# Performance work log

Hardware: AMD Instinct MI355X
Metric: run time of the kernel (lower is better)

## Reference

```python
import jax, jax.numpy as jnp
import numpy as np

N_NODES = 50000
N_EDGES = 800000
F_IN = 64
HID = 128
N_GRAPHS = 64
F_OUT = 1
NEG_SLOPE = 0.2


def _glorot(key, shape):
    fan_in, fan_out = shape[0], shape[-1]
    s = jnp.sqrt(6.0 / (fan_in + fan_out))
    return jax.random.uniform(key, shape, jnp.float32, -s, s)


def setup_inputs() -> dict:
    key = jax.random.key(0)
    ks = jax.random.split(key, 24)
    inp = {
        "x": jax.random.normal(ks[0], (N_NODES, F_IN), jnp.float32),
        "edge_index": jax.random.randint(ks[1], (2, N_EDGES), 0, N_NODES, jnp.int32),
        "edge_weight": jax.random.uniform(ks[2], (N_EDGES, 1), jnp.float32),
        "batch": jnp.sort(jax.random.randint(ks[3], (N_NODES,), 0, N_GRAPHS, jnp.int32)),
        # GATv2Conv layer 1 (heads=1): lin_l, lin_r (with bias), lin_edge (no bias), att, out-bias
        "W1l": _glorot(ks[4], (F_IN, HID)), "b1l": jnp.zeros((HID,), jnp.float32),
        "W1r": _glorot(ks[5], (F_IN, HID)), "b1r": jnp.zeros((HID,), jnp.float32),
        "We1": _glorot(ks[6], (1, HID)),
        "att1": _glorot(ks[7], (HID, 1))[:, 0],
        "bias1": jnp.zeros((HID,), jnp.float32),
        # GATv2Conv layer 2
        "W2l": _glorot(ks[8], (HID, HID)), "b2l": jnp.zeros((HID,), jnp.float32),
        "W2r": _glorot(ks[9], (HID, HID)), "b2r": jnp.zeros((HID,), jnp.float32),
        "We2": _glorot(ks[10], (1, HID)),
        "att2": _glorot(ks[11], (HID, 1))[:, 0],
        "bias2": jnp.zeros((HID,), jnp.float32),
        # final Linear
        "Wlin": _glorot(ks[12], (HID, F_OUT)),
        "blin": jnp.zeros((F_OUT,), jnp.float32),
    }
    return inp


def gatv2_layer(x, src, dst, eattr, Wl, bl, Wr, br, We, att, bias):
    n = x.shape[0]
    # add_self_loops=True with edge_attr fill_value='mean'
    loop = jnp.arange(n, dtype=src.dtype)
    src = jnp.concatenate([src, loop])
    dst = jnp.concatenate([dst, loop])
    mean_attr = jnp.mean(eattr, axis=0, keepdims=True)  # [1, edge_dim]
    eattr = jnp.concatenate([eattr, jnp.broadcast_to(mean_attr, (n, eattr.shape[1]))])
    xl = x @ Wl + bl            # [N, HID] source transform
    xr = x @ Wr + br            # [N, HID] dest transform
    ee = eattr @ We             # [E', HID] edge embedding
    m = jax.nn.leaky_relu(xl[src] + xr[dst] + ee, NEG_SLOPE)  # [E', HID]
    logits = m @ att            # [E']
    # per-destination softmax (every node has a self loop, so no empty segments)
    lmax = jax.ops.segment_max(logits, dst, num_segments=n)
    w = jnp.exp(logits - lmax[dst])
    denom = jax.ops.segment_sum(w, dst, num_segments=n)
    alpha = w / denom[dst]
    out = jax.ops.segment_sum(xl[src] * alpha[:, None], dst, num_segments=n)
    return out + bias


def reference(x, edge_index, edge_weight, batch,
              W1l, b1l, W1r, b1r, We1, att1, bias1,
              W2l, b2l, W2r, b2r, We2, att2, bias2,
              Wlin, blin):
    src, dst = edge_index[0], edge_index[1]
    h = jax.nn.relu(gatv2_layer(x, src, dst, edge_weight, W1l, b1l, W1r, b1r, We1, att1, bias1))
    h = jax.nn.relu(gatv2_layer(h, src, dst, edge_weight, W2l, b2l, W2r, b2r, We2, att2, bias2))
    # global_mean_pool over graph assignment
    sums = jax.ops.segment_sum(h, batch, num_segments=N_GRAPHS)
    cnt = jax.ops.segment_sum(jnp.ones((h.shape[0],), h.dtype), batch, num_segments=N_GRAPHS)
    pooled = sums / jnp.maximum(cnt, 1.0)[:, None]
    return pooled @ Wlin + blin  # [N_GRAPHS, F_OUT]
```

## Files before the change

### kernel.cpp

```cpp
#include <hip/hip_runtime.h>

#define NN 50000
#define NE 800000
#define EP (NE + NN)
#define HID 128
#define FIN 64
#define NG 64
#define SLOPE 0.2f
#define NB 49

typedef unsigned short ushort_t;
typedef unsigned int uint_t;
typedef __attribute__((ext_vector_type(8))) short bf16x8;
typedef __attribute__((ext_vector_type(4))) float f32x4;

__device__ __forceinline__ float wred_sum(float v) {
  for (int off = 32; off; off >>= 1) v += __shfl_xor(v, off);
  return v;
}
__device__ __forceinline__ ushort_t f2bf(float f) {
  uint_t b = __float_as_uint(f);
  b += 0x7fffu + ((b >> 16) & 1u);
  return (ushort_t)(b >> 16);
}
__device__ __forceinline__ float bf2f(ushort_t u) {
  return __uint_as_float((uint_t)u << 16);
}

__global__ void k_prep(const float* __restrict__ x, ushort_t* __restrict__ x16,
                       const float* __restrict__ W1l, ushort_t* __restrict__ WP1l,
                       const float* __restrict__ W1r, ushort_t* __restrict__ WP1r,
                       const float* __restrict__ W2l, ushort_t* __restrict__ WP2l,
                       const float* __restrict__ W2r, ushort_t* __restrict__ WP2r) {
  int i = blockIdx.x * blockDim.x + threadIdx.x;
  const int R0 = NN * FIN / 4;
  const int RS = FIN * HID;
  const int RB = HID * HID;
  if (i < R0) {
    float4 v = *(const float4*)(x + (size_t)i * 4);
    ushort4 u;
    u.x = f2bf(v.x); u.y = f2bf(v.y); u.z = f2bf(v.z); u.w = f2bf(v.w);
    *(ushort4*)(x16 + (size_t)i * 4) = u;
    return;
  }
  i -= R0;
  if (i < RS) {
    int k = i / HID, nn = i % HID;
    WP1l[((size_t)(k >> 5) * HID + nn) * 32 + (k & 31)] = f2bf(W1l[i]);
    return;
  }
  i -= RS;
  if (i < RS) {
    int k = i / HID, nn = i % HID;
    WP1r[((size_t)(k >> 5) * HID + nn) * 32 + (k & 31)] = f2bf(W1r[i]);
    return;
  }
  i -= RS;
  if (i < RB) {
    int k = i / HID, nn = i % HID;
    WP2l[((size_t)(k >> 5) * HID + nn) * 32 + (k & 31)] = f2bf(W2l[i]);
    return;
  }
  i -= RB;
  if (i < RB) {
    int k = i / HID, nn = i % HID;
    WP2r[((size_t)(k >> 5) * HID + nn) * 32 + (k & 31)] = f2bf(W2r[i]);
  }
}

__global__ void k_hist2(const int* __restrict__ edst, const float* __restrict__ ew,
                        int* __restrict__ counts, float* __restrict__ meansum) {
  int tid = blockIdx.x * blockDim.x + threadIdx.x;
  int stride = gridDim.x * blockDim.x;
  float s = 0.f;
  for (int i = tid; i < NE; i += stride) {
    atomicAdd(&counts[edst[i]], 1);
    s += ew[i];
  }
  s = wred_sum(s);
  if ((threadIdx.x & 63) == 0) atomicAdd(meansum, s);
}

__global__ __launch_bounds__(1024) void k_scan1(const int* __restrict__ counts,
                                                int* __restrict__ starts,
                                                int* __restrict__ bsum) {
  __shared__ int wsum[16];
  __shared__ int woff[16];
  int t = threadIdx.x, lane = t & 63, w = t >> 6;
  int i = blockIdx.x * 1024 + t;
  int v = (i < NN) ? counts[i] + 1 : 0;
  int sc = v;
  #pragma unroll
  for (int d = 1; d < 64; d <<= 1) {
    int u = __shfl_up(sc, d);
    if (lane >= d) sc += u;
  }
  if (lane == 63) wsum[w] = sc;
  __syncthreads();
  if (w == 0 && lane < 16) {
    int x = wsum[lane];
    #pragma unroll
    for (int d = 1; d < 16; d <<= 1) {
      int u = __shfl_up(x, d);
      if (lane >= d) x += u;
    }
    woff[lane] = x;
  }
  __syncthreads();
  int waveoff = (w == 0) ? 0 : woff[w - 1];
  if (i < NN) starts[i] = waveoff + sc - v;
  if (t == 1023) bsum[blockIdx.x] = woff[15];
}

__global__ void k_scan2(int* __restrict__ bsum, int* __restrict__ starts) {
  int t = threadIdx.x;
  int v = (t < NB) ? bsum[t] : 0;
  int sc = v;
  #pragma unroll
  for (int d = 1; d < 64; d <<= 1) {
    int u = __shfl_up(sc, d);
    if (t >= d) sc += u;
  }
  if (t < NB) bsum[t] = sc - v;
  if (t == 0) starts[NN] = EP;
}

__global__ __launch_bounds__(1024) void k_scan3(int* __restrict__ starts,
                                                const int* __restrict__ bsum,
                                                int* __restrict__ counts,
                                                const int* __restrict__ batch,
                                                int* __restrict__ gs) {
  int i = blockIdx.x * 1024 + threadIdx.x;
  if (i < NN) {
    starts[i] += bsum[blockIdx.x];
    counts[i] = 0;
    int b = batch[i];
    if (i == 0) {
      for (int g = 0; g <= b; ++g) gs[g] = 0;
    }
    int bn = (i + 1 < NN) ? batch[i + 1] : NG;
    for (int g = b + 1; g <= bn; ++g) gs[g] = i + 1;
  }
}

__global__ void k_scatter(const int* __restrict__ esrc, const int* __restrict__ edst,
                          const float* __restrict__ ew, const float* __restrict__ meansum,
                          const int* __restrict__ starts, int* __restrict__ cursor,
                          int2* __restrict__ emeta) {
  float mw = meansum[0] * (1.0f / NE);
  int tid = blockIdx.x * blockDim.x + threadIdx.x;
  int stride = gridDim.x * blockDim.x;
  for (int i = tid; i < EP; i += stride) {
    int s, d; float wv;
    if (i < NE) { s = esrc[i]; d = edst[i]; wv = ew[i]; }
    else        { s = d = i - NE; wv = mw; }
    int pos = starts[d] + atomicAdd(&cursor[d], 1);
    emeta[pos] = make_int2(s, __float_as_int(wv));
  }
}

template <int K>
__global__ __launch_bounds__(256) void k_gemmM(const ushort_t* __restrict__ A16,
                                               const ushort_t* __restrict__ WPl,
                                               const float* __restrict__ bl,
                                               const ushort_t* __restrict__ WPr,
                                               const float* __restrict__ br,
                                               ushort_t* __restrict__ xlout,
                                               float* __restrict__ xrout, int n) {
  int t = threadIdx.x;
  int wave = t >> 6, lane = t & 63;
  int m = lane & 15, kb = lane >> 4;
  int row0 = blockIdx.x * 64 + wave * 16;
  int ra = min(row0 + m, n - 1);
  f32x4 acc[16];
  #pragma unroll
  for (int i = 0; i < 16; ++i) acc[i] = (f32x4)(0.f);
  #pragma unroll
  for (int kt = 0; kt < K / 32; ++kt) {
    bf16x8 a = *(const bf16x8*)(A16 + (size_t)ra * K + kt * 32 + kb * 8);
    #pragma unroll
    for (int nf = 0; nf < 8; ++nf) {
      bf16x8 bfr = *(const bf16x8*)(WPl + ((size_t)kt * HID + nf * 16 + m) * 32 + kb * 8);
      acc[nf] = __builtin_amdgcn_mfma_f32_16x16x32_bf16(a, bfr, acc[nf], 0, 0, 0);
    }
    #pragma unroll
    for (int nf = 0; nf < 8; ++nf) {
      bf16x8 bfr = *(const bf16x8*)(WPr + ((size_t)kt * HID + nf * 16 + m) * 32 + kb * 8);
      acc[8 + nf] = __builtin_amdgcn_mfma_f32_16x16x32_bf16(a, bfr, acc[8 + nf], 0, 0, 0);
    }
  }
  #pragma unroll
  for (int nf = 0; nf < 8; ++nf) {
    int col = nf * 16 + m;
    float bbl = bl[col], bbr = br[col];
    #pragma unroll
    for (int j = 0; j < 4; ++j) {
      int r = row0 + kb * 4 + j;
      if (r < n) {
        xlout[(size_t)r * HID + col] = f2bf(acc[nf][j] + bbl);
        xrout[(size_t)r * HID + col] = acc[8 + nf][j] + bbr;
      }
    }
  }
}

__global__ __launch_bounds__(256, 2) void k_fused(const ushort_t* __restrict__ xl16,
                                                  const float* __restrict__ xr,
                                                  const int2* __restrict__ emeta,
                                                  const int* __restrict__ starts,
                                                  const float* __restrict__ We,
                                                  const float* __restrict__ att,
                                                  const float* __restrict__ bias,
                                                  ushort_t* __restrict__ hout) {
  int node = blockIdx.x * (blockDim.x >> 6) + (threadIdx.x >> 6);
  int lane = threadIdx.x & 63;
  if (node >= NN) return;
  int hl = lane & 31;
  int half = lane >> 5;
  int s0 = starts[node], s1 = starts[node + 1];
  int f = hl * 4;
  float4 xro = *(const float4*)(xr + (size_t)node * HID + f);
  float4 we  = *(const float4*)(We + f);
  float4 at  = *(const float4*)(att + f);

  int emy = 8 * half + ((hl >> 2) & 7);
  bool b4 = (hl & 16) != 0;
  bool b3 = (hl & 8) != 0;
  bool b2 = (hl & 4) != 0;

  float ssum = 0.f;
  float4 acc = make_float4(0.f, 0.f, 0.f, 0.f);

  auto loadset = [&](uint2 (&g)[8], float (&p)[8], int i0) {
    int base = i0 + 8 * half;
    #pragma unroll
    for (int k = 0; k < 8; ++k) {
      int idx = min(base + k, s1 - 1);
      int2 em = emeta[idx];
      p[k] = __int_as_float(em.y);
      g[k] = *(const uint2*)(xl16 + (size_t)em.x * HID + f);
    }
  };
  auto process = [&](uint2 (&g)[8], float (&p)[8], int i0) {
    #pragma unroll
    for (int k = 0; k < 8; ++k) {
      float wk = p[k];
      float t0 = __uint_as_float(g[k].x << 16)          + xro.x + wk * we.x;
      float t1 = __uint_as_float(g[k].x & 0xffff0000u)  + xro.y + wk * we.y;
      float t2 = __uint_as_float(g[k].y << 16)          + xro.z + wk * we.z;
      float t3 = __uint_as_float(g[k].y & 0xffff0000u)  + xro.w + wk * we.w;
      t0 = t0 > 0.f ? t0 : SLOPE * t0;
      t1 = t1 > 0.f ? t1 : SLOPE * t1;
      t2 = t2 > 0.f ? t2 : SLOPE * t2;
      t3 = t3 > 0.f ? t3 : SLOPE * t3;
      p[k] = t0 * at.x + t1 * at.y + t2 * at.z + t3 * at.w;
    }
    float sdv, rcv;
    float q0, q1, q2, q3;
    sdv = b4 ? p[0] : p[4]; rcv = __shfl_xor(sdv, 16, 32); q0 = (b4 ? p[4] : p[0]) + rcv;
    sdv = b4 ? p[1] : p[5]; rcv = __shfl_xor(sdv, 16, 32); q1 = (b4 ? p[5] : p[1]) + rcv;
    sdv = b4 ? p[2] : p[6]; rcv = __shfl_xor(sdv, 16, 32); q2 = (b4 ? p[6] : p[2]) + rcv;
    sdv = b4 ? p[3] : p[7]; rcv = __shfl_xor(sdv, 16, 32); q3 = (b4 ? p[7] : p[3]) + rcv;
    float r0, r1;
    sdv = b3 ? q0 : q2; rcv = __shfl_xor(sdv, 8, 32); r0 = (b3 ? q2 : q0) + rcv;
    sdv = b3 ? q1 : q3; rcv = __shfl_xor(sdv, 8, 32); r1 = (b3 ? q3 : q1) + rcv;
    sdv = b2 ? r0 : r1; rcv = __shfl_xor(sdv, 4, 32);
    float lg = (b2 ? r1 : r0) + rcv;
    lg += __shfl_xor(lg, 1, 32);
    lg += __shfl_xor(lg, 2, 32);
    float w = (i0 + emy < s1) ? __expf(lg) : 0.f;
    ssum += w;
    #pragma unroll
    for (int k = 0; k < 8; ++k) {
      float wk = __shfl(w, k << 2, 32);
      acc.x += wk * __uint_as_float(g[k].x << 16);
      acc.y += wk * __uint_as_float(g[k].x & 0xffff0000u);
      acc.z += wk * __uint_as_float(g[k].y << 16);
      acc.w += wk * __uint_as_float(g[k].y & 0xffff0000u);
    }
  };

  uint2 gA[8], gB[8];
  float pA[8], pB[8];
  int i0 = s0;
  loadset(gA, pA, i0);
  while (true) {
    int i1 = i0 + 16;
    bool haveB = (i1 < s1);
    if (haveB) loadset(gB, pB, i1);
    process(gA, pA, i0);
    if (!haveB) break;
    int i2 = i1 + 16;
    bool haveA = (i2 < s1);
    if (haveA) loadset(gA, pA, i2);
    process(gB, pB, i1);
    if (!haveA) break;
    i0 = i2;
  }

  acc.x += __shfl_xor(acc.x, 32);
  acc.y += __shfl_xor(acc.y, 32);
  acc.z += __shfl_xor(acc.z, 32);
  acc.w += __shfl_xor(acc.w, 32);
  float st = wred_sum(ssum) * 0.25f;
  float inv = 1.0f / st;
  if (half == 0) {
    float4 bb = *(const float4*)(bias + f);
    ushort4 u;
    u.x = f2bf(fmaxf(acc.x * inv + bb.x, 0.f));
    u.y = f2bf(fmaxf(acc.y * inv + bb.y, 0.f));
    u.z = f2bf(fmaxf(acc.z * inv + bb.z, 0.f));
    u.w = f2bf(fmaxf(acc.w * inv + bb.w, 0.f));
    *(ushort4*)(hout + (size_t)node * HID + f) = u;
  }
}

__global__ __launch_bounds__(256) void k_pool(const ushort_t* __restrict__ h,
                                              const int* __restrict__ gs,
                                              const float* __restrict__ Wlin,
                                              const float* __restrict__ blin,
                                              float* __restrict__ out) {
  __shared__ float red[256];
  int g = blockIdx.x;
  int t = threadIdx.x;
  int f = t & 127;
  int half = t >> 7;
  int n0 = gs[g], n1 = gs[g + 1];
  float s0 = 0.f, s1 = 0.f, s2 = 0.f, s3 = 0.f;
  int n = n0 + half;
  for (; n + 6 < n1; n += 8) {
    s0 += bf2f(h[(size_t)n * HID + f]);
    s1 += bf2f(h[(size_t)(n + 2) * HID + f]);
    s2 += bf2f(h[(size_t)(n + 4) * HID + f]);
    s3 += bf2f(h[(size_t)(n + 6) * HID + f]);
  }
  for (; n < n1; n += 2) s0 += bf2f(h[(size_t)n * HID + f]);
  red[t] = (s0 + s1) + (s2 + s3);
  __syncthreads();
  if (t < 128) {
    float pooled = red[t] + red[t + 128];
    float cnt = (float)max(n1 - n0, 1);
    red[t] = (pooled / cnt) * Wlin[f];
  }
  __syncthreads();
  if (t < 64) {
    float v = red[t] + red[t + 64];
    v = wred_sum(v);
    if (t == 0) out[g] = v + blin[0];
  }
}

extern "C" void kernel_launch(void* const* d_in, const int* in_sizes, int n_in,
                              void* d_out, int out_size, void* d_ws, size_t ws_size,
                              hipStream_t stream) {
  const float* x     = (const float*)d_in[0];
  const int*   ei    = (const int*)d_in[1];
  const float* ew    = (const float*)d_in[2];
  const int*   batch = (const int*)d_in[3];
  const float* W1l = (const float*)d_in[4];
  const float* b1l = (const float*)d_in[5];
  const float* W1r = (const float*)d_in[6];
  const float* b1r = (const float*)d_in[7];
  const float* We1 = (const float*)d_in[8];
  const float* at1 = (const float*)d_in[9];
  const float* bi1 = (const float*)d_in[10];
  const float* W2l = (const float*)d_in[11];
  const float* b2l = (const float*)d_in[12];
  const float* W2r = (const float*)d_in[13];
  const float* b2r = (const float*)d_in[14];
  const float* We2 = (const float*)d_in[15];
  const float* at2 = (const float*)d_in[16];
  const float* bi2 = (const float*)d_in[17];
  const float* Wlin = (const float*)d_in[18];
  const float* blin = (const float*)d_in[19];

  float* ws = (float*)d_ws;
  size_t o = 0;
  float*    xr    = ws + o; o += (size_t)NN * HID;
  ushort_t* xl16  = (ushort_t*)(ws + o); o += (size_t)NN * HID / 2;
  ushort_t* hb16  = (ushort_t*)(ws + o); o += (size_t)NN * HID / 2;
  ushort_t* x16   = (ushort_t*)(ws + o); o += (size_t)NN * FIN / 2;
  ushort_t* WP1l  = (ushort_t*)(ws + o); o += (size_t)FIN * HID / 2;
  ushort_t* WP1r  = (ushort_t*)(ws + o); o += (size_t)FIN * HID / 2;
  ushort_t* WP2l  = (ushort_t*)(ws + o); o += (size_t)HID * HID / 2;
  ushort_t* WP2r  = (ushort_t*)(ws + o); o += (size_t)HID * HID / 2;
  int2*     emeta = (int2*)(ws + o); o += (size_t)2 * EP;
  int*      starts = (int*)(ws + o); o += NN + 1;
  int*      gs     = (int*)(ws + o); o += NG + 1;
  int*      bsum   = (int*)(ws + o); o += NB;
  size_t zoff = o;
  int*      counts  = (int*)(ws + o); o += NN;
  float*    meansum = ws + o; o += 1;
  size_t zero_bytes = (o - zoff) * sizeof(float);

  hipMemsetAsync(counts, 0, zero_bytes, stream);

  const int PREP = NN * FIN / 4 + 2 * FIN * HID + 2 * HID * HID;
  k_prep<<<(PREP + 255) / 256, 256, 0, stream>>>(x, x16, W1l, WP1l, W1r, WP1r,
                                                 W2l, WP2l, W2r, WP2r);

  k_hist2<<<1024, 256, 0, stream>>>(ei + NE, ew, counts, meansum);
  k_scan1<<<NB, 1024, 0, stream>>>(counts, starts, bsum);
  k_scan2<<<1, 64, 0, stream>>>(bsum, starts);
  k_scan3<<<NB, 1024, 0, stream>>>(starts, bsum, counts, batch, gs);
  k_scatter<<<1024, 256, 0, stream>>>(ei, ei + NE, ew, meansum, starts, counts,
                                      emeta);

  int gb  = (NN + 63) / 64;
  int nbn = (NN + 3) / 4;

  k_gemmM<FIN><<<gb, 256, 0, stream>>>(x16, WP1l, b1l, WP1r, b1r, xl16, xr, NN);
  k_fused<<<nbn, 256, 0, stream>>>(xl16, xr, emeta, starts, We1, at1, bi1, hb16);
  k_gemmM<HID><<<gb, 256, 0, stream>>>(hb16, WP2l, b2l, WP2r, b2r, xl16, xr, NN);
  k_fused<<<nbn, 256, 0, stream>>>(xl16, xr, emeta, starts, We2, at2, bi2, hb16);
  k_pool<<<NG, 256, 0, stream>>>(hb16, gs, Wlin, blin, (float*)d_out);
}
```

Measured before the change: 396.9 us.

## Merge prep with histogram, fold block scan into scan3, simplify fused gather loop

The edge histogram kernel is merged into the prep kernel as extra blocks, and the single-block scan of block sums is folded into every scan3 block. Together these remove two kernel launches and the gaps between them. Separately, the fused attention kernel drops its manual double-buffered gather loop for a plain loop and raises the launch-bounds occupancy hint from 2 to 4, trading explicit load/compute overlap for lower register use and more resident waves. scan3 now recomputes the small block-sum scan in each block, which is redundant but cheap.

```diff
diff --git a/kernel.cpp b/kernel.cpp
--- a/kernel.cpp
+++ b/kernel.cpp
@@ -8,6 +8,9 @@
 #define NG 64
 #define SLOPE 0.2f
 #define NB 49
+#define PREPN (NN * FIN / 4 + 2 * FIN * HID + 2 * HID * HID)
+#define PREPB ((PREPN + 255) / 256)
+#define HISTB 1024
 
 typedef unsigned short ushort_t;
 typedef unsigned int uint_t;
@@ -31,7 +34,21 @@
                        const float* __restrict__ W1l, ushort_t* __restrict__ WP1l,
                        const float* __restrict__ W1r, ushort_t* __restrict__ WP1r,
                        const float* __restrict__ W2l, ushort_t* __restrict__ WP2l,
-                       const float* __restrict__ W2r, ushort_t* __restrict__ WP2r) {
+                       const float* __restrict__ W2r, ushort_t* __restrict__ WP2r,
+                       const int* __restrict__ edst, const float* __restrict__ ew,
+                       int* __restrict__ counts, float* __restrict__ meansum) {
+  if (blockIdx.x >= PREPB) {
+    int tid = (blockIdx.x - PREPB) * blockDim.x + threadIdx.x;
+    int stride = HISTB * 256;
+    float s = 0.f;
+    for (int i = tid; i < NE; i += stride) {
+      atomicAdd(&counts[edst[i]], 1);
+      s += ew[i];
+    }
+    s = wred_sum(s);
+    if ((threadIdx.x & 63) == 0) atomicAdd(meansum, s);
+    return;
+  }
   int i = blockIdx.x * blockDim.x + threadIdx.x;
   const int R0 = NN * FIN / 4;
   const int RS = FIN * HID;
@@ -66,19 +83,6 @@
     int k = i / HID, nn = i % HID;
     WP2r[((size_t)(k >> 5) * HID + nn) * 32 + (k & 31)] = f2bf(W2r[i]);
   }
-}
-
-__global__ void k_hist2(const int* __restrict__ edst, const float* __restrict__ ew,
-                        int* __restrict__ counts, float* __restrict__ meansum) {
-  int tid = blockIdx.x * blockDim.x + threadIdx.x;
-  int stride = gridDim.x * blockDim.x;
-  float s = 0.f;
-  for (int i = tid; i < NE; i += stride) {
-    atomicAdd(&counts[edst[i]], 1);
-    s += ew[i];
-  }
-  s = wred_sum(s);
-  if ((threadIdx.x & 63) == 0) atomicAdd(meansum, s);
 }
 
 __global__ __launch_bounds__(1024) void k_scan1(const int* __restrict__ counts,
@@ -112,30 +116,31 @@
   if (t == 1023) bsum[blockIdx.x] = woff[15];
 }
 
-__global__ void k_scan2(int* __restrict__ bsum, int* __restrict__ starts) {
-  int t = threadIdx.x;
-  int v = (t < NB) ? bsum[t] : 0;
-  int sc = v;
-  #pragma unroll
-  for (int d = 1; d < 64; d <<= 1) {
-    int u = __shfl_up(sc, d);
-    if (t >= d) sc += u;
-  }
-  if (t < NB) bsum[t] = sc - v;
-  if (t == 0) starts[NN] = EP;
-}
-
 __global__ __launch_bounds__(1024) void k_scan3(int* __restrict__ starts,
                                                 const int* __restrict__ bsum,
                                                 int* __restrict__ counts,
                                                 const int* __restrict__ batch,
                                                 int* __restrict__ gs) {
-  int i = blockIdx.x * 1024 + threadIdx.x;
+  __shared__ int boff;
+  int t = threadIdx.x;
+  if (t < 64) {
+    int v = (t < NB) ? bsum[t] : 0;
+    int sc = v;
+    #pragma unroll
+    for (int d = 1; d < 64; d <<= 1) {
+      int u = __shfl_up(sc, d);
+      if (t >= d) sc += u;
+    }
+    if (t == (int)blockIdx.x) boff = sc - v;
+  }
+  __syncthreads();
+  int i = blockIdx.x * 1024 + t;
   if (i < NN) {
-    starts[i] += bsum[blockIdx.x];
+    starts[i] += boff;
     counts[i] = 0;
     int b = batch[i];
     if (i == 0) {
+      starts[NN] = EP;
       for (int g = 0; g <= b; ++g) gs[g] = 0;
     }
     int bn = (i + 1 < NN) ? batch[i + 1] : NG;
@@ -204,7 +209,7 @@
   }
 }
 
-__global__ __launch_bounds__(256, 2) void k_fused(const ushort_t* __restrict__ xl16,
+__global__ __launch_bounds__(256, 4) void k_fused(const ushort_t* __restrict__ xl16,
                                                   const float* __restrict__ xr,
                                                   const int2* __restrict__ emeta,
                                                   const int* __restrict__ starts,
@@ -231,8 +236,10 @@
   float ssum = 0.f;
   float4 acc = make_float4(0.f, 0.f, 0.f, 0.f);
 
-  auto loadset = [&](uint2 (&g)[8], float (&p)[8], int i0) {
+  for (int i0 = s0; i0 < s1; i0 += 16) {
     int base = i0 + 8 * half;
+    uint2 g[8];
+    float p[8];
     #pragma unroll
     for (int k = 0; k < 8; ++k) {
       int idx = min(base + k, s1 - 1);
@@ -240,8 +247,6 @@
       p[k] = __int_as_float(em.y);
       g[k] = *(const uint2*)(xl16 + (size_t)em.x * HID + f);
     }
-  };
-  auto process = [&](uint2 (&g)[8], float (&p)[8], int i0) {
     #pragma unroll
     for (int k = 0; k < 8; ++k) {
       float wk = p[k];
@@ -278,26 +283,7 @@
       acc.z += wk * __uint_as_float(g[k].y << 16);
       acc.w += wk * __uint_as_float(g[k].y & 0xffff0000u);
     }
-  };
-
-  uint2 gA[8], gB[8];
-  float pA[8], pB[8];
-  int i0 = s0;
-  loadset(gA, pA, i0);
-  while (true) {
-    int i1 = i0 + 16;
-    bool haveB = (i1 < s1);
-    if (haveB) loadset(gB, pB, i1);
-    process(gA, pA, i0);
-    if (!haveB) break;
-    int i2 = i1 + 16;
-    bool haveA = (i2 < s1);
-    if (haveA) loadset(gA, pA, i2);
-    process(gB, pB, i1);
-    if (!haveA) break;
-    i0 = i2;
-  }
-
+  }
   acc.x += __shfl_xor(acc.x, 32);
   acc.y += __shfl_xor(acc.y, 32);
   acc.z += __shfl_xor(acc.z, 32);
@@ -395,13 +381,11 @@
 
   hipMemsetAsync(counts, 0, zero_bytes, stream);
 
-  const int PREP = NN * FIN / 4 + 2 * FIN * HID + 2 * HID * HID;
-  k_prep<<<(PREP + 255) / 256, 256, 0, stream>>>(x, x16, W1l, WP1l, W1r, WP1r,
-                                                 W2l, WP2l, W2r, WP2r);
-
-  k_hist2<<<1024, 256, 0, stream>>>(ei + NE, ew, counts, meansum);
+  k_prep<<<PREPB + HISTB, 256, 0, stream>>>(x, x16, W1l, WP1l, W1r, WP1r,
+                                            W2l, WP2l, W2r, WP2r,
+                                            ei + NE, ew, counts, meansum);
+
   k_scan1<<<NB, 1024, 0, stream>>>(counts, starts, bsum);
-  k_scan2<<<1, 64, 0, stream>>>(bsum, starts);
   k_scan3<<<NB, 1024, 0, stream>>>(starts, bsum, counts, batch, gs);
   k_scatter<<<1024, 256, 0, stream>>>(ei, ei + NE, ew, meansum, starts, counts,
                                       emeta);
```

After: 387.8 us, median of 2. 2.3% less time.
